# Kernel tuning notes

Hardware: AMD Instinct MI355X
Metric: run time of the kernel (lower is better)

## Reference

```python
import jax, jax.numpy as jnp
import numpy as np

B, S, D = 2, 2048, 1024
M = 2048          # d_mlp
E = 8             # num_experts
TOP_K = 2


def setup_inputs() -> dict:
    key = jax.random.key(0)
    ks = jax.random.split(key, 5)
    std = 0.02
    return {
        "residual": jax.random.normal(ks[0], (B, S, D), jnp.float32),
        "W_router": jax.random.normal(ks[1], (D, E), jnp.float32) * std,
        "W_gate": jax.random.normal(ks[2], (E, D, M), jnp.float32) * std,
        "b_gate": jnp.zeros((E, M), jnp.float32),
        "W_up": jax.random.normal(ks[3], (E, D, M), jnp.float32) * std,
        "b_up": jnp.zeros((E, M), jnp.float32),
        "W_out": jax.random.normal(ks[4], (E, M, D), jnp.float32) * std,
        "b_out": jnp.zeros((E, D), jnp.float32),
    }


def reference(residual, W_router, W_gate, b_gate, W_up, b_up, W_out, b_out):
    # --- router: softmax over experts, top-k selection, renormalize ---
    router_logits = jnp.einsum('bsd,de->bse', residual, W_router)
    router_probs = jax.nn.softmax(router_logits, axis=-1)
    top_k_probs, top_k_idx = jax.lax.top_k(router_probs, TOP_K)          # [B,S,K]
    top_k_probs = top_k_probs / (jnp.sum(top_k_probs, -1, keepdims=True) + 1e-8)
    # per-expert combine weight [B,S,E]; top-k indices are unique per token
    one_hot = jax.nn.one_hot(top_k_idx, E, dtype=residual.dtype)          # [B,S,K,E]
    expert_weights = jnp.einsum('bsk,bske->bse', top_k_probs, one_hot)
    # --- each expert runs dense SwiGLU MLP on the FULL batch (compute-then-mask, as in source) ---
    gate = jax.nn.silu(jnp.einsum('bsd,edm->ebsm', residual, W_gate) + b_gate[:, None, None, :])
    up = jnp.einsum('bsd,edm->ebsm', residual, W_up) + b_up[:, None, None, :]
    hidden = gate * up                                                    # [E,B,S,M]
    expert_out = jnp.einsum('ebsm,emd->ebsd', hidden, W_out) + b_out[:, None, None, :]
    # --- weighted combine (weights are zero for non-selected experts) ---
    output = jnp.einsum('bse,ebsd->bsd', expert_weights, expert_out)
    return output
```

## Files before the change

### kernel.cpp

```cpp
#include <hip/hip_runtime.h>
#include <cstdint>
#include <cstddef>

#define TT 4096
#define DD 1024
#define MM 2048
#define EE 8
#define NPAIR 8192

typedef unsigned short u16;
typedef __bf16 bf16x8 __attribute__((ext_vector_type(8)));
typedef float f32x4 __attribute__((ext_vector_type(4)));
typedef u16 u16x8 __attribute__((ext_vector_type(8)));
typedef __attribute__((address_space(3))) void* lds_vp;
typedef __attribute__((address_space(1))) const void* gbl_cvp;

__device__ __forceinline__ void async16(u16* l, const u16* g) {
  __builtin_amdgcn_global_load_lds((gbl_cvp)(const void*)g, (lds_vp)(void*)l, 16, 0, 0);
}

#define VMCNT6() asm volatile("s_waitcnt vmcnt(6)" ::: "memory")
#define VMCNT4() asm volatile("s_waitcnt vmcnt(4)" ::: "memory")
#define VMCNT0() asm volatile("s_waitcnt vmcnt(0)" ::: "memory")
#define BARR() do { asm volatile("" ::: "memory"); __builtin_amdgcn_s_barrier(); asm volatile("" ::: "memory"); } while (0)

__device__ __forceinline__ u16 f2bf(float f) {
  uint32_t u = __builtin_bit_cast(uint32_t, f);
  u += 0x7fffu + ((u >> 16) & 1u);
  return (u16)(u >> 16);
}
__device__ __forceinline__ float bf2f(u16 h) {
  uint32_t u = ((uint32_t)h) << 16;
  return __builtin_bit_cast(float, u);
}

__global__ void router_kernel(const float* __restrict__ X, const float* __restrict__ Wr,
                              int* __restrict__ tok_idx, float* __restrict__ wpair,
                              u16* __restrict__ Xbf) {
  int wave = threadIdx.x >> 6;
  int lane = threadIdx.x & 63;
  int t = blockIdx.x * 4 + wave;
  const float4* x4 = (const float4*)(X + (size_t)t * DD);
  float acc[EE];
#pragma unroll
  for (int e = 0; e < EE; e++) acc[e] = 0.f;
#pragma unroll
  for (int i = 0; i < 4; i++) {
    float4 xv = x4[i * 64 + lane];
    ushort4 o;
    o.x = f2bf(xv.x); o.y = f2bf(xv.y); o.z = f2bf(xv.z); o.w = f2bf(xv.w);
    *(ushort4*)&Xbf[(size_t)t * DD + (size_t)(i * 64 + lane) * 4] = o;
    const float4* wr4 = (const float4*)(Wr + (size_t)(i * 256 + lane * 4) * EE);
    float xs[4] = {xv.x, xv.y, xv.z, xv.w};
#pragma unroll
    for (int c = 0; c < 4; c++) {
      float4 wa = wr4[c * 2 + 0];
      float4 wb = wr4[c * 2 + 1];
      acc[0] += xs[c] * wa.x; acc[1] += xs[c] * wa.y;
      acc[2] += xs[c] * wa.z; acc[3] += xs[c] * wa.w;
      acc[4] += xs[c] * wb.x; acc[5] += xs[c] * wb.y;
      acc[6] += xs[c] * wb.z; acc[7] += xs[c] * wb.w;
    }
  }
#pragma unroll
  for (int off = 32; off > 0; off >>= 1)
#pragma unroll
    for (int e = 0; e < EE; e++) acc[e] += __shfl_xor(acc[e], off);
  if (lane == 0) {
    float mx = acc[0];
#pragma unroll
    for (int e = 1; e < EE; e++) mx = fmaxf(mx, acc[e]);
    float p[EE], s = 0.f;
#pragma unroll
    for (int e = 0; e < EE; e++) { p[e] = __expf(acc[e] - mx); s += p[e]; }
    float inv = 1.f / s;
#pragma unroll
    for (int e = 0; e < EE; e++) p[e] *= inv;
    int i0 = 0;
#pragma unroll
    for (int e = 1; e < EE; e++) if (p[e] > p[i0]) i0 = e;
    int i1 = (i0 == 0) ? 1 : 0;
#pragma unroll
    for (int e = 0; e < EE; e++) if (e != i0 && p[e] > p[i1]) i1 = e;
    float denom = p[i0] + p[i1] + 1e-8f;
    tok_idx[t * 2 + 0] = i0;
    tok_idx[t * 2 + 1] = i1;
    wpair[t * 2 + 0] = p[i0] / denom;
    wpair[t * 2 + 1] = p[i1] / denom;
  }
}

__global__ void bucket_kernel(const int* __restrict__ tok_idx, int* __restrict__ offsets,
                              int* __restrict__ bucket) {
  __shared__ int lcnt[EE];
  __shared__ int lcur[EE];
  int tid = threadIdx.x;
  int lane = tid & 63;
  if (tid < EE) lcnt[tid] = 0;
  __syncthreads();
  {
    int cnt[EE];
#pragma unroll
    for (int k = 0; k < EE; k++) cnt[k] = 0;
    for (int i = tid; i < NPAIR; i += 1024) {
      int e = tok_idx[i];
#pragma unroll
      for (int k = 0; k < EE; k++) {
        unsigned long long m = __ballot(e == k);
        cnt[k] += __popcll(m);
      }
    }
    if (lane == 0) {
#pragma unroll
      for (int k = 0; k < EE; k++)
        if (cnt[k]) atomicAdd(&lcnt[k], cnt[k]);
    }
  }
  __syncthreads();
  if (tid == 0) {
    int s = 0;
    for (int e = 0; e < EE; e++) {
      offsets[e] = s;
      lcur[e] = s;
      s += lcnt[e];
    }
    offsets[EE] = s;
  }
  __syncthreads();
  for (int i = tid; i < NPAIR; i += 1024) {
    int e = tok_idx[i];
    int pos = 0;
#pragma unroll
    for (int k = 0; k < EE; k++) {
      unsigned long long m = __ballot(e == k);
      int c = __popcll(m);
      if (c) {
        int leader = (int)__ffsll((long long)m) - 1;
        int base = 0;
        if (lane == leader) base = atomicAdd(&lcur[k], c);
        base = __shfl(base, leader);
        if (e == k) pos = base + __popcll(m & ((1ull << lane) - 1ull));
      }
    }
    bucket[pos] = i;
  }
}

__global__ __launch_bounds__(256)
void transpose_cvt(const float* __restrict__ in, u16* __restrict__ out, int R, int C) {
  __shared__ float tile[64][65];
  int e = blockIdx.z;
  const float* I = in + (size_t)e * R * C;
  u16* O = out + (size_t)e * R * C;
  int c0 = blockIdx.x * 64, r0 = blockIdx.y * 64;
  int t = threadIdx.x;
  {
    int cq = t & 15;
    int rb = t >> 4;
#pragma unroll
    for (int i = 0; i < 4; i++) {
      int r = rb + i * 16;
      float4 v = *(const float4*)&I[(size_t)(r0 + r) * C + c0 + cq * 4];
      tile[cq * 4 + 0][r] = v.x;
      tile[cq * 4 + 1][r] = v.y;
      tile[cq * 4 + 2][r] = v.z;
      tile[cq * 4 + 3][r] = v.w;
    }
  }
  __syncthreads();
  {
    int rseg = (t & 7) * 8;
    int cc = t >> 3;
#pragma unroll
    for (int i = 0; i < 2; i++) {
      int c = cc + i * 32;
      u16x8 o;
#pragma unroll
      for (int k = 0; k < 8; k++) o[k] = f2bf(tile[c][rseg + k]);
      *(u16x8*)&O[(size_t)(c0 + c) * R + r0 + rseg] = o;
    }
  }
}

__device__ __forceinline__ bool tile_map(const int* __restrict__ offsets, int x,
                                         int& expert, int& row0, int& rows) {
  expert = -1;
#pragma unroll 1
  for (int e = 0; e < EE; e++) {
    int o0 = offsets[e], o1 = offsets[e + 1];
    int nt = (o1 - o0 + 127) >> 7;
    if (x < nt) { expert = e; row0 = o0 + (x << 7); rows = min(128, o1 - row0); return true; }
    x -= nt;
  }
  return false;
}

template <int NTLOG2>
__device__ __forceinline__ void grid_decode(int bid, int& rt, int& n0) {
  int xcd = bid & 7, slot = bid >> 3;
  rt = xcd * 9 + (slot >> NTLOG2);
  n0 = (slot & ((1 << NTLOG2) - 1)) * 128;
}


__global__ __launch_bounds__(256, 2)
void moe_gemm_gu(const u16* __restrict__ Xbf, const u16* __restrict__ WtG,
                 const u16* __restrict__ WtU, const float* __restrict__ bgate,
                 const float* __restrict__ bup, u16* __restrict__ Hws,
                 const int* __restrict__ offsets, const int* __restrict__ bucket) {
  int rt, n0;
  grid_decode<4>(blockIdx.x, rt, n0);
  int expert, row0, rows;
  if (!tile_map(offsets, rt, expert, row0, rows)) return;

  __shared__ u16 Alds[3 * 128 * 32];
  __shared__ u16 Glds[3 * 128 * 32];
  __shared__ u16 Ulds[3 * 128 * 32];

  int tid = threadIdx.x;
  int wave = tid >> 6, lane = tid & 63;
  int wm = wave >> 1, wn = wave & 1;
  int quad = lane >> 4, l15 = lane & 15;
  int swz = ((lane & 3) ^ ((lane >> 3) & 3)) * 8;
  int rp  = (quad ^ ((l15 >> 1) & 3)) * 8;

  long arow0, arow1;
  {
    int r0l = wave * 32 + (lane >> 2);
    int rr0 = min(r0l, rows - 1);
    int rr1 = min(r0l + 16, rows - 1);
    arow0 = (long)(bucket[row0 + rr0] >> 1) * DD;
    arow1 = (long)(bucket[row0 + rr1] >> 1) * DD;
  }
  const u16* A0 = Xbf + arow0 + swz;
  const u16* A1 = Xbf + arow1 + swz;
  size_t bo = (size_t)expert * MM * DD + (size_t)n0 * DD
            + (long)(wave * 32 + (lane >> 2)) * DD + swz;
  const u16* G0 = WtG + bo; const u16* G1 = G0 + 16 * DD;
  const u16* U0 = WtU + bo; const u16* U1 = U0 + 16 * DD;

  int sb0 = (wave * 32) * 32, sb1 = (wave * 32 + 16) * 32;

  f32x4 accG[4][4], accU[4][4];
#pragma unroll
  for (int i = 0; i < 4; i++)
#pragma unroll
    for (int j = 0; j < 4; j++) { accG[i][j] = (f32x4){0,0,0,0}; accU[i][j] = (f32x4){0,0,0,0}; }

  auto stage = [&](int b) {
    int bo2 = b * (128 * 32);
    async16(&Alds[bo2 + sb0], A0); async16(&Alds[bo2 + sb1], A1);
    async16(&Glds[bo2 + sb0], G0); async16(&Glds[bo2 + sb1], G1);
    async16(&Ulds[bo2 + sb0], U0); async16(&Ulds[bo2 + sb1], U1);
    A0 += 32; A1 += 32; G0 += 32; G1 += 32; U0 += 32; U1 += 32;
  };

  auto compute = [&](int b) {
    int ro = b * (128 * 32);
    bf16x8 af[4], bf[4];
#pragma unroll
    for (int i = 0; i < 4; i++) {
      af[i] = *(const bf16x8*)&Alds[ro + (wm * 64 + i * 16 + l15) * 32 + rp];
      bf[i] = *(const bf16x8*)&Glds[ro + (wn * 64 + i * 16 + l15) * 32 + rp];
    }
    __builtin_amdgcn_s_setprio(1);
#pragma unroll
    for (int i = 0; i < 4; i++)
#pragma unroll
      for (int j = 0; j < 4; j++)
        accG[i][j] = __builtin_amdgcn_mfma_f32_16x16x32_bf16(af[i], bf[j], accG[i][j], 0, 0, 0);
    __builtin_amdgcn_s_setprio(0);
#pragma unroll
    for (int i = 0; i < 4; i++)
      bf[i] = *(const bf16x8*)&Ulds[ro + (wn * 64 + i * 16 + l15) * 32 + rp];
    __builtin_amdgcn_s_setprio(1);
#pragma unroll
    for (int i = 0; i < 4; i++)
#pragma unroll
      for (int j = 0; j < 4; j++)
        accU[i][j] = __builtin_amdgcn_mfma_f32_16x16x32_bf16(af[i], bf[j], accU[i][j], 0, 0, 0);
    __builtin_amdgcn_s_setprio(0);
  };

  constexpr int NT = DD / 32;
  stage(0);
  stage(1);
  int br = 0, bs = 2;
#pragma unroll 1
  for (int t = 0; t < NT - 2; ++t) {
    VMCNT6();
    BARR();
    stage(bs);
    compute(br);
    bs = br; br = (br + 1 == 3) ? 0 : br + 1;
  }
  VMCNT6(); BARR(); compute(br); br = (br + 1 == 3) ? 0 : br + 1;
  VMCNT0(); BARR(); compute(br);

#pragma unroll
  for (int i = 0; i < 4; i++) {
    int lrb = wm * 64 + i * 16 + quad * 4;
#pragma unroll
    for (int j = 0; j < 4; j++) {
      int gc = n0 + wn * 64 + j * 16 + l15;
      float bg = bgate[expert * MM + gc];
      float bu = bup[expert * MM + gc];
#pragma unroll
      for (int r = 0; r < 4; r++) {
        int lr = lrb + r;
        if (lr < rows) {
          int grow = row0 + lr;
          float g = accG[i][j][r] + bg;
          float u = accU[i][j][r] + bu;
          float sg = g / (1.f + __expf(-g));
          Hws[(size_t)grow * MM + gc] = f2bf(sg * u);
        }
      }
    }
  }
}

__global__ __launch_bounds__(256, 3)
void moe_gemm_out(const u16* __restrict__ Hmat, const u16* __restrict__ WtO,
                  const float* __restrict__ bias, float* __restrict__ Ypart,
                  const int* __restrict__ offsets, const int* __restrict__ bucket,
                  const float* __restrict__ wpair) {
  int rt, n0;
  grid_decode<3>(blockIdx.x, rt, n0);
  int expert, row0, rows;
  if (!tile_map(offsets, rt, expert, row0, rows)) return;

  __shared__ u16 Alds[3 * 128 * 32];
  __shared__ u16 Blds[3 * 128 * 32];

  int tid = threadIdx.x;
  int wave = tid >> 6, lane = tid & 63;
  int wm = wave >> 1, wn = wave & 1;
  int quad = lane >> 4, l15 = lane & 15;
  int swz = ((lane & 3) ^ ((lane >> 3) & 3)) * 8;
  int rp  = (quad ^ ((l15 >> 1) & 3)) * 8;

  long arow0, arow1;
  {
    int r0l = wave * 32 + (lane >> 2);
    int rr0 = min(r0l, rows - 1);
    int rr1 = min(r0l + 16, rows - 1);
    arow0 = (long)(row0 + rr0) * MM;
    arow1 = (long)(row0 + rr1) * MM;
  }
  const u16* A0 = Hmat + arow0 + swz;
  const u16* A1 = Hmat + arow1 + swz;
  const u16* B0 = WtO + (size_t)expert * DD * MM + (size_t)n0 * MM
                + (long)(wave * 32 + (lane >> 2)) * MM + swz;
  const u16* B1 = B0 + 16 * MM;

  int sb0 = (wave * 32) * 32, sb1 = (wave * 32 + 16) * 32;

  f32x4 acc[4][4];
#pragma unroll
  for (int i = 0; i < 4; i++)
#pragma unroll
    for (int j = 0; j < 4; j++) acc[i][j] = (f32x4){0, 0, 0, 0};

  auto stage = [&](int b) {
    int bo2 = b * (128 * 32);
    async16(&Alds[bo2 + sb0], A0); async16(&Alds[bo2 + sb1], A1);
    async16(&Blds[bo2 + sb0], B0); async16(&Blds[bo2 + sb1], B1);
    A0 += 32; A1 += 32; B0 += 32; B1 += 32;
  };

  auto compute = [&](int b) {
    int ro = b * (128 * 32);
    bf16x8 af[4], bf[4];
#pragma unroll
    for (int i = 0; i < 4; i++) {
      af[i] = *(const bf16x8*)&Alds[ro + (wm * 64 + i * 16 + l15) * 32 + rp];
      bf[i] = *(const bf16x8*)&Blds[ro + (wn * 64 + i * 16 + l15) * 32 + rp];
    }
    __builtin_amdgcn_s_setprio(1);
#pragma unroll
    for (int i = 0; i < 4; i++)
#pragma unroll
      for (int j = 0; j < 4; j++)
        acc[i][j] = __builtin_amdgcn_mfma_f32_16x16x32_bf16(af[i], bf[j], acc[i][j], 0, 0, 0);
    __builtin_amdgcn_s_setprio(0);
  };

  constexpr int NT = MM / 32;
  stage(0);
  stage(1);
  int br = 0, bs = 2;
#pragma unroll 1
  for (int t = 0; t < NT - 2; ++t) {
    VMCNT4();
    BARR();
    stage(bs);
    compute(br);
    bs = br; br = (br + 1 == 3) ? 0 : br + 1;
  }
  VMCNT4(); BARR(); compute(br); br = (br + 1 == 3) ? 0 : br + 1;
  VMCNT0(); BARR(); compute(br);

#pragma unroll
  for (int i = 0; i < 4; i++) {
    int lrb = wm * 64 + i * 16 + quad * 4;
#pragma unroll
    for (int j = 0; j < 4; j++) {
      int gc = n0 + wn * 64 + j * 16 + l15;
      float bv = bias[expert * DD + gc];
#pragma unroll
      for (int r = 0; r < 4; r++) {
        int lr = lrb + r;
        if (lr < rows) {
          int grow = row0 + lr;
          int p = bucket[grow];
          float w = wpair[p];
          Ypart[(size_t)p * DD + gc] = w * (acc[i][j][r] + bv);
        }
      }
    }
  }
}

__global__ void combine_kernel(const float* __restrict__ Ypart, float* __restrict__ out) {
  int i = blockIdx.x * 256 + threadIdx.x;
  int t = i >> 8;
  int c4 = i & 255;
  const float4* y0 = (const float4*)(Ypart + (size_t)(2 * t) * DD) + c4;
  const float4* y1 = (const float4*)(Ypart + (size_t)(2 * t + 1) * DD) + c4;
  float4 a = *y0, b = *y1;
  float4 o;
  o.x = a.x + b.x; o.y = a.y + b.y; o.z = a.z + b.z; o.w = a.w + b.w;
  ((float4*)out)[i] = o;
}

extern "C" void kernel_launch(void* const* d_in, const int* in_sizes, int n_in,
                              void* d_out, int out_size, void* d_ws, size_t ws_size,
                              hipStream_t stream) {
  const float* residual = (const float*)d_in[0];
  const float* W_router = (const float*)d_in[1];
  const float* W_gate   = (const float*)d_in[2];
  const float* b_gate   = (const float*)d_in[3];
  const float* W_up     = (const float*)d_in[4];
  const float* b_up     = (const float*)d_in[5];
  const float* W_out    = (const float*)d_in[6];
  const float* b_out    = (const float*)d_in[7];
  float* out = (float*)d_out;

  char* ws = (char*)d_ws;
  int*   tok_idx = (int*)(ws + 0);
  float* wpair   = (float*)(ws + 32768);
  int*   offsets = (int*)(ws + 65536);
  int*   bucket  = (int*)(ws + 65536 + 512);
  u16*   Xbf  = (u16*)(ws + 131072);
  u16*   WtG  = Xbf + (size_t)TT * DD;
  u16*   WtU  = WtG + (size_t)EE * MM * DD;
  u16*   WtO  = WtU + (size_t)EE * MM * DD;
  u16*   Hws  = WtO + (size_t)EE * DD * MM;
  float* Ypart = (float*)(Hws + (size_t)NPAIR * MM);

  router_kernel<<<dim3(TT / 4), dim3(256), 0, stream>>>(residual, W_router, tok_idx, wpair, Xbf);
  bucket_kernel<<<dim3(1), dim3(1024), 0, stream>>>(tok_idx, offsets, bucket);
  transpose_cvt<<<dim3(MM / 64, DD / 64, EE), dim3(256), 0, stream>>>(W_gate, WtG, DD, MM);
  transpose_cvt<<<dim3(MM / 64, DD / 64, EE), dim3(256), 0, stream>>>(W_up,   WtU, DD, MM);
  transpose_cvt<<<dim3(DD / 64, MM / 64, EE), dim3(256), 0, stream>>>(W_out,  WtO, MM, DD);
  moe_gemm_gu<<<dim3(8 * 9 * 16), dim3(256), 0, stream>>>(Xbf, WtG, WtU, b_gate, b_up, Hws, offsets, bucket);
  moe_gemm_out<<<dim3(8 * 9 * 8), dim3(256), 0, stream>>>(Hws, WtO, b_out, Ypart, offsets, bucket, wpair);
  combine_kernel<<<dim3(TT * DD / 4 / 256), dim3(256), 0, stream>>>(Ypart, out);
}
```

Measured before the change: 468.0 us.

## Fuse combine into out-GEMM via atomics, merge transposes, reorder tile decode

Removes the separate combine kernel and the Ypart buffer. The output is zeroed inside the router kernel, and the out-GEMM epilogue atomically adds each token's two weighted expert contributions into the output. The three weight transpose launches become a single launch that picks its matrix from blockIdx.z. The grid decode changes from row-tile-major to n-tile-major ordering within each XCD. This saves a full fp32 write and re-read of the pair buffer plus several launches, at the cost of atomic float adds and a summation order that is no longer deterministic.

```diff
diff --git a/kernel.cpp b/kernel.cpp
--- a/kernel.cpp
+++ b/kernel.cpp
@@ -36,7 +36,14 @@
 
 __global__ void router_kernel(const float* __restrict__ X, const float* __restrict__ Wr,
                               int* __restrict__ tok_idx, float* __restrict__ wpair,
-                              u16* __restrict__ Xbf) {
+                              u16* __restrict__ Xbf, float* __restrict__ out) {
+  {
+    int idx = blockIdx.x * 256 + threadIdx.x;
+    float4 z4 = {0.f, 0.f, 0.f, 0.f};
+    float4* o4 = (float4*)out;
+#pragma unroll
+    for (int k = 0; k < 4; k++) o4[idx + k * (TT / 4) * 256] = z4;
+  }
   int wave = threadIdx.x >> 6;
   int lane = threadIdx.x & 63;
   int t = blockIdx.x * 4 + wave;
@@ -147,12 +154,22 @@
 }
 
 __global__ __launch_bounds__(256)
-void transpose_cvt(const float* __restrict__ in, u16* __restrict__ out, int R, int C) {
+void transpose_all(const float* __restrict__ Gf, const float* __restrict__ Uf,
+                   const float* __restrict__ Of, u16* __restrict__ tG,
+                   u16* __restrict__ tU, u16* __restrict__ tO) {
   __shared__ float tile[64][65];
-  int e = blockIdx.z;
+  int z = blockIdx.z;
+  const float* in; u16* out; int R, C, shift;
+  int e;
+  if (z < 8)       { in = Gf; out = tG; R = DD; C = MM; e = z;      shift = 5; }
+  else if (z < 16) { in = Uf; out = tU; R = DD; C = MM; e = z - 8;  shift = 5; }
+  else             { in = Of; out = tO; R = MM; C = DD; e = z - 16; shift = 4; }
+  int tidx = blockIdx.y * 32 + blockIdx.x;
+  int cx = tidx & ((1 << shift) - 1);
+  int cy = tidx >> shift;
   const float* I = in + (size_t)e * R * C;
   u16* O = out + (size_t)e * R * C;
-  int c0 = blockIdx.x * 64, r0 = blockIdx.y * 64;
+  int c0 = cx * 64, r0 = cy * 64;
   int t = threadIdx.x;
   {
     int cq = t & 15;
@@ -195,11 +212,10 @@
   return false;
 }
 
-template <int NTLOG2>
 __device__ __forceinline__ void grid_decode(int bid, int& rt, int& n0) {
   int xcd = bid & 7, slot = bid >> 3;
-  rt = xcd * 9 + (slot >> NTLOG2);
-  n0 = (slot & ((1 << NTLOG2) - 1)) * 128;
+  rt = xcd * 9 + slot % 9;
+  n0 = (slot / 9) * 128;
 }
 
 
@@ -209,7 +225,7 @@
                  const float* __restrict__ bup, u16* __restrict__ Hws,
                  const int* __restrict__ offsets, const int* __restrict__ bucket) {
   int rt, n0;
-  grid_decode<4>(blockIdx.x, rt, n0);
+  grid_decode(blockIdx.x, rt, n0);
   int expert, row0, rows;
   if (!tile_map(offsets, rt, expert, row0, rows)) return;
 
@@ -322,11 +338,11 @@
 
 __global__ __launch_bounds__(256, 3)
 void moe_gemm_out(const u16* __restrict__ Hmat, const u16* __restrict__ WtO,
-                  const float* __restrict__ bias, float* __restrict__ Ypart,
+                  const float* __restrict__ bias, float* __restrict__ out,
                   const int* __restrict__ offsets, const int* __restrict__ bucket,
                   const float* __restrict__ wpair) {
   int rt, n0;
-  grid_decode<3>(blockIdx.x, rt, n0);
+  grid_decode(blockIdx.x, rt, n0);
   int expert, row0, rows;
   if (!tile_map(offsets, rt, expert, row0, rows)) return;
 
@@ -415,23 +431,11 @@
           int grow = row0 + lr;
           int p = bucket[grow];
           float w = wpair[p];
-          Ypart[(size_t)p * DD + gc] = w * (acc[i][j][r] + bv);
+          atomicAdd(&out[(size_t)(p >> 1) * DD + gc], w * (acc[i][j][r] + bv));
         }
       }
     }
   }
-}
-
-__global__ void combine_kernel(const float* __restrict__ Ypart, float* __restrict__ out) {
-  int i = blockIdx.x * 256 + threadIdx.x;
-  int t = i >> 8;
-  int c4 = i & 255;
-  const float4* y0 = (const float4*)(Ypart + (size_t)(2 * t) * DD) + c4;
-  const float4* y1 = (const float4*)(Ypart + (size_t)(2 * t + 1) * DD) + c4;
-  float4 a = *y0, b = *y1;
-  float4 o;
-  o.x = a.x + b.x; o.y = a.y + b.y; o.z = a.z + b.z; o.w = a.w + b.w;
-  ((float4*)out)[i] = o;
 }
 
 extern "C" void kernel_launch(void* const* d_in, const int* in_sizes, int n_in,
@@ -457,14 +461,10 @@
   u16*   WtU  = WtG + (size_t)EE * MM * DD;
   u16*   WtO  = WtU + (size_t)EE * MM * DD;
   u16*   Hws  = WtO + (size_t)EE * DD * MM;
-  float* Ypart = (float*)(Hws + (size_t)NPAIR * MM);
-
-  router_kernel<<<dim3(TT / 4), dim3(256), 0, stream>>>(residual, W_router, tok_idx, wpair, Xbf);
+
+  router_kernel<<<dim3(TT / 4), dim3(256), 0, stream>>>(residual, W_router, tok_idx, wpair, Xbf, out);
   bucket_kernel<<<dim3(1), dim3(1024), 0, stream>>>(tok_idx, offsets, bucket);
-  transpose_cvt<<<dim3(MM / 64, DD / 64, EE), dim3(256), 0, stream>>>(W_gate, WtG, DD, MM);
-  transpose_cvt<<<dim3(MM / 64, DD / 64, EE), dim3(256), 0, stream>>>(W_up,   WtU, DD, MM);
-  transpose_cvt<<<dim3(DD / 64, MM / 64, EE), dim3(256), 0, stream>>>(W_out,  WtO, MM, DD);
+  transpose_all<<<dim3(32, 16, 24), dim3(256), 0, stream>>>(W_gate, W_up, W_out, WtG, WtU, WtO);
   moe_gemm_gu<<<dim3(8 * 9 * 16), dim3(256), 0, stream>>>(Xbf, WtG, WtU, b_gate, b_up, Hws, offsets, bucket);
-  moe_gemm_out<<<dim3(8 * 9 * 8), dim3(256), 0, stream>>>(Hws, WtO, b_out, Ypart, offsets, bucket, wpair);
-  combine_kernel<<<dim3(TT * DD / 4 / 256), dim3(256), 0, stream>>>(Ypart, out);
-}
+  moe_gemm_out<<<dim3(8 * 9 * 8), dim3(256), 0, stream>>>(Hws, WtO, b_out, out, offsets, bucket, wpair);
+}
```

New measurement: 493.5 us. +5.5%, slower.
